# Performance work log

Measured on AMD Instinct MI355X. Metric: run time of the kernel, lower is better.

The kernel has to match this reference:

```python
import jax, jax.numpy as jnp
import numpy as np

N = 50000      # nodes
CI = 256       # multiplicity of irreps_in  (256x0e + 256x1o)
CH = 128       # multiplicity of irreps_hidden (128x0e + 128x1o)
INV_SQRT3 = 0.5773502691896258  # CG norm for 1o x 1o -> 0e (dot)


def _split(x, C):
    # e3nn layout: [scalars (C), vectors (C*3, per-channel m-contiguous)]
    return x[:, :C], x[:, C:].reshape(x.shape[0], C, 3)


def _normgate(s, v, w1, b1, w2, b2):
    # QHNet NormGate: concat(scalars, per-channel vector norms) -> MLP -> gates
    norms = jnp.sqrt(jnp.sum(v * v, axis=-1))                      # [N, Cv]
    g = jax.nn.silu(jnp.concatenate([s, norms], 1) @ w1 + b1) @ w2 + b2
    Cs = s.shape[1]
    return jax.nn.silu(g[:, :Cs]), v * g[:, Cs:, None]


def _o3linear(s, v, W0, b0, W1):
    # per-irrep block-diagonal linear, e3nn fan-in normalization; bias only on 0e
    inv = 1.0 / np.sqrt(s.shape[1]).astype(np.float32)
    return s @ W0 * inv + b0, jnp.einsum('nui,uh->nhi', v, W1) * inv


def _forward(x, fcl1_w, fcl1_b, fcl2_w, fcl2_b, fcr1_w, fcr1_b, fcr2_w, fcr2_b,
             fcp1_w, fcp1_b, fcp2_w, fcp2_b, Wl0, bl0, Wl1, Wr0, br0, Wr1,
             Wp0, bp0, Wp1, w_ss, w_sv, w_vs, w_vv):
    s, v = _split(x, CI)                                           # [N,CI],[N,CI,3]
    # left / right branches: NormGate -> o3.Linear (irreps_in -> irreps_hidden)
    ls, lv = _normgate(s, v, fcl1_w, fcl1_b, fcl2_w, fcl2_b)
    ls, lv = _o3linear(ls, lv, Wl0, bl0, Wl1)                      # [N,CH],[N,CH,3]
    rs, rv = _normgate(s, v, fcr1_w, fcr1_b, fcr2_w, fcr2_b)
    rs, rv = _o3linear(rs, rv, Wr0, br0, Wr1)
    # channelwise ('uuu') CG tensor product with internal per-channel weights
    # paths: 0e*0e->0e, 1o.1o->0e, 0e*1o->1o, 1o*0e->1o
    s_a = w_ss * ls * rs
    s_b = w_vv * jnp.sum(lv * rv, -1) * INV_SQRT3
    v_a = w_sv[None, :, None] * ls[:, :, None] * rv
    v_b = w_vs[None, :, None] * lv * rs[:, :, None]
    tp_s = jnp.concatenate([s_a, s_b], 1)                          # [N, 2*CH]
    tp_v = jnp.concatenate([v_a, v_b], 1)                          # [N, 2*CH, 3]
    # residual update (irreps_tp_out == irreps_in by construction)
    tp_s = tp_s + s
    tp_v = tp_v + v
    # output gate + projection to hidden irreps
    ps, pv = _normgate(tp_s, tp_v, fcp1_w, fcp1_b, fcp2_w, fcp2_b)
    ps, pv = _o3linear(ps, pv, Wp0, bp0, Wp1)                      # [N,CH],[N,CH,3]
    return jnp.concatenate([ps, pv.reshape(pv.shape[0], -1)], 1)   # [N, 4*CH]


def setup_inputs():
    key = jax.random.key(0)
    ks = jax.random.split(key, 24)
    M = 2 * CI  # total multiplicity of irreps_in / irreps_tp_out (NormGate fc width)

    def lin(k, fi, fo):
        return jax.random.normal(k, (fi, fo), jnp.float32) / np.sqrt(fi)

    inp = {"x": jax.random.normal(ks[0], (N, 4 * CI), jnp.float32)}
    i = 1
    for nm in ["fcl", "fcr", "fcp"]:
        inp[nm + "1_w"] = lin(ks[i], M, M); i += 1
        inp[nm + "1_b"] = jnp.zeros((M,), jnp.float32)
        inp[nm + "2_w"] = lin(ks[i], M, M); i += 1
        inp[nm + "2_b"] = jnp.zeros((M,), jnp.float32)
    for nm in ["Wl", "Wr", "Wp"]:
        inp[nm + "0"] = jax.random.normal(ks[i], (CI, CH), jnp.float32); i += 1
        inp["b" + nm[1] + "0"] = jnp.zeros((CH,), jnp.float32)
        inp[nm + "1"] = jax.random.normal(ks[i], (CI, CH), jnp.float32); i += 1
    for nm in ["w_ss", "w_sv", "w_vs", "w_vv"]:
        inp[nm] = jax.random.normal(ks[i], (CH,), jnp.float32); i += 1
    return inp


def reference(x, fcl1_w, fcl1_b, fcl2_w, fcl2_b, fcr1_w, fcr1_b, fcr2_w, fcr2_b,
              fcp1_w, fcp1_b, fcp2_w, fcp2_b, Wl0, bl0, Wl1, Wr0, br0, Wr1,
              Wp0, bp0, Wp1, w_ss, w_sv, w_vs, w_vv):
    return _forward(x, fcl1_w, fcl1_b, fcl2_w, fcl2_b, fcr1_w, fcr1_b, fcr2_w,
                    fcr2_b, fcp1_w, fcp1_b, fcp2_w, fcp2_b, Wl0, bl0, Wl1, Wr0,
                    br0, Wr1, Wp0, bp0, Wp1, w_ss, w_sv, w_vs, w_vv)
```

## Files before the change

kernel.cpp:

```cpp
#include <hip/hip_runtime.h>
#include <cstddef>

#define NN 50000
#define NP 50048
#define RT 391

typedef unsigned short u16;
typedef __attribute__((ext_vector_type(8))) short bf16x8;
typedef __attribute__((ext_vector_type(4))) float f32x4;

__device__ __forceinline__ float bf2f(u16 h){
  union { unsigned u; float f; } x; x.u = ((unsigned)h) << 16; return x.f;
}
__device__ __forceinline__ u16 f2bf(float f){
  union { float f; unsigned u; } x; x.f = f;
  unsigned r = x.u + 0x7fffu + ((x.u >> 16) & 1u);
  return (u16)(r >> 16);
}
__device__ __forceinline__ float silu_f(float v){
  return v / (1.f + __expf(-v));
}
__device__ __forceinline__ void gll16(const u16* g, u16* l){
  __builtin_amdgcn_global_load_lds(
      (const __attribute__((address_space(1))) unsigned int*)g,
      (__attribute__((address_space(3))) unsigned int*)l, 16, 0, 0);
}
__device__ __forceinline__ int xcd_swz(int hw, int nblk){
  int q = nblk >> 3, r = nblk & 7;
  int xcd = hw & 7, j = hw >> 3;
  return (xcd < r ? xcd*(q+1) : r*(q+1) + (xcd - r)*q) + j;
}
#define SWZ(row) (((row) >> 1) & 3)

__global__ __launch_bounds__(256)
void k_wt(const float* b0,const float* b1,const float* b2,const float* b3,
          const float* b4,const float* b5,
          const float* s0,const float* s1,const float* s2,const float* s3,
          const float* s4,const float* s5, u16* __restrict__ dst){
  __shared__ float t[64][68];
  const int m = blockIdx.y;
  const bool big = (m < 6);
  const int K = big ? 512 : 256, C = big ? 512 : 128;
  const int tC = C >> 6;
  const int tiles = (K >> 6) * tC;
  if((int)blockIdx.x >= tiles) return;
  const int k0 = ((int)blockIdx.x / tC) << 6, c0 = ((int)blockIdx.x % tC) << 6;
  const float* src = m==0?b0:m==1?b1:m==2?b2:m==3?b3:m==4?b4:m==5?b5:
                     m==6?s0:m==7?s1:m==8?s2:m==9?s3:m==10?s4:s5;
  u16* d = dst + (big ? (size_t)m*262144 : (size_t)(6*262144) + (size_t)(m-6)*32768);
  const int tr = threadIdx.x >> 2, tc = (threadIdx.x & 3) << 4;
  const float* sp = src + (size_t)(k0 + tr)*C + c0 + tc;
#pragma unroll
  for(int j=0;j<16;j+=4) *(f32x4*)&t[tr][tc + j] = *(const f32x4*)(sp + j);
  __syncthreads();
  u16* dp = d + (size_t)(c0 + tr)*K + k0 + tc;
#pragma unroll
  for(int j=0;j<16;j++) dp[j] = f2bf(t[tc + j][tr]);
}

__global__ __launch_bounds__(256)
void k_prep(const float* __restrict__ x, u16* __restrict__ A0,
            u16* __restrict__ XVp){
  const int n = blockIdx.x;
  const int t = threadIdx.x;
  u16* row = A0 + (size_t)n * 512;
  u16* xv  = XVp + (size_t)n * 768;
  if(n >= NN){
    row[t] = 0; row[256 + t] = 0;
    xv[t] = 0; xv[256 + t] = 0; xv[512 + t] = 0;
    return;
  }
  const float* xr = x + (size_t)n * 1024;
  row[t] = f2bf(xr[t]);
  float a = xr[256 + 3*t], b = xr[256 + 3*t + 1], c = xr[256 + 3*t + 2];
  row[256 + t] = f2bf(sqrtf(a*a + b*b + c*c));
  xv[t] = f2bf(a); xv[256 + t] = f2bf(b); xv[512 + t] = f2bf(c);
}

template<int K, int RING>
__device__ __forceinline__ void gemm_core(const u16* __restrict__ A, int lda,
                                          const u16* __restrict__ Bt, int ldb,
                                          u16* lds, f32x4 acc[4][4]){
  constexpr int NT = K / 32;
  static_assert(NT >= RING, "");
  const int tid  = threadIdx.x;
  const int lane = tid & 63;
  const int wid  = tid >> 6;
  const int wm = (wid >> 1) << 6;
  const int wn = (wid & 1) << 6;
  const int lr = lane & 15;
  const int lh = lane >> 4;
#pragma unroll
  for(int mi=0;mi<4;mi++)
#pragma unroll
    for(int ni=0;ni<4;ni++) acc[mi][ni] = (f32x4)(0.f);

  const int r0 = tid >> 2, s0 = tid & 3, r1 = (tid + 256) >> 2;
  const u16* agA0 = A  + (size_t)r0*lda + (size_t)((s0 ^ SWZ(r0)) * 8);
  const u16* agA1 = A  + (size_t)r1*lda + (size_t)((s0 ^ SWZ(r1)) * 8);
  const u16* agB0 = Bt + (size_t)r0*ldb + (size_t)((s0 ^ SWZ(r0)) * 8);
  const u16* agB1 = Bt + (size_t)r1*ldb + (size_t)((s0 ^ SWZ(r1)) * 8);

#define STAGE(b, k0)                                         \
  { u16* lbase = lds + (size_t)(b) * 8192;                   \
    gll16(agA0 + (k0), lbase + tid*8);                       \
    gll16(agA1 + (k0), lbase + (tid+256)*8);                 \
    gll16(agB0 + (k0), lbase + 4096 + tid*8);                \
    gll16(agB1 + (k0), lbase + 4096 + (tid+256)*8); }

#pragma unroll
  for(int p=0;p<RING-1;p++) STAGE(p, p*32)

  int cur = 0, nxt = RING - 1;
  for(int kt = 0; kt < NT; ++kt){
    if constexpr      (RING == 5) asm volatile("s_waitcnt vmcnt(12)" ::: "memory");
    else if constexpr (RING == 4) asm volatile("s_waitcnt vmcnt(8)"  ::: "memory");
    else                          asm volatile("s_waitcnt vmcnt(4)"  ::: "memory");
    __builtin_amdgcn_s_barrier();
    {
      int kf = kt + RING - 1; if(kf > NT-1) kf = NT-1;
      STAGE(nxt, kf*32)
    }
    const u16* la = lds + (size_t)cur * 8192;
    const u16* lb = la + 4096;
    bf16x8 af[4], bv[4];
#pragma unroll
    for(int i=0;i<4;i++){
      const int ra = wm + i*16 + lr;
      af[i] = *(const bf16x8*)(la + ra*32 + ((lh ^ SWZ(ra)) * 8));
      const int rb = wn + i*16 + lr;
      bv[i] = *(const bf16x8*)(lb + rb*32 + ((lh ^ SWZ(rb)) * 8));
    }
    __builtin_amdgcn_s_setprio(1);
#pragma unroll
    for(int mi=0;mi<4;mi++)
#pragma unroll
      for(int ni=0;ni<4;ni++)
        acc[mi][ni] = __builtin_amdgcn_mfma_f32_16x16x32_bf16(
                          af[mi], bv[ni], acc[mi][ni], 0, 0, 0);
    __builtin_amdgcn_s_setprio(0);
    cur = (cur == RING-1) ? 0 : cur + 1;
    nxt = (nxt == RING-1) ? 0 : nxt + 1;
  }
#undef STAGE
  asm volatile("s_waitcnt vmcnt(0)" ::: "memory");
  __builtin_amdgcn_s_barrier();
}

__device__ __forceinline__ void cstage_write(u16* lds, int rl, int cl, float v){
  const int b = ((rl << 8) + (cl << 1)) ^ ((rl & 7) << 4);
  *(u16*)((char*)lds + b) = f2bf(v);
}
__device__ __forceinline__ bf16x8 cstage_read(const u16* lds, int rl, int cl){
  const int b = ((rl << 8) + (cl << 1)) ^ ((rl & 7) << 4);
  return *(const bf16x8*)((const char*)lds + b);
}

template<int EPI, int NZ>
__global__ __launch_bounds__(256, 3)
void k_fc(const u16* __restrict__ Al, const u16* __restrict__ Ar,
          const u16* __restrict__ Btl, const u16* __restrict__ Btr,
          const float* __restrict__ bl, const float* __restrict__ br_,
          u16* __restrict__ ol, u16* __restrict__ orr,
          const u16* __restrict__ gsrc){
  __shared__ u16 lds[24576];
  const int nblk = RT * 4 * NZ;
  const int L = xcd_swz(blockIdx.x, nblk);
  int rowTileI, colTileI, z;
  if(NZ == 2){ rowTileI = L >> 3; int sub = L & 7; colTileI = sub >> 1; z = sub & 1; }
  else       { rowTileI = L >> 2; colTileI = L & 3; z = 0; }
  const u16* A  = z ? Ar  : Al;
  const u16* Bt = z ? Btr : Btl;
  const float* bias = z ? br_ : bl;
  u16* o = z ? orr : ol;
  const int tileRow = rowTileI << 7;
  const int colTile = colTileI << 7;
  f32x4 acc[4][4];
  gemm_core<512,3>(A + (size_t)tileRow*512, 512, Bt + (size_t)colTile*512, 512,
                   lds, acc);
  const int tid = threadIdx.x, lane = tid & 63, wid = tid >> 6;
  const int wm=(wid>>1)<<6, wn=(wid&1)<<6, lr=lane&15, lh=lane>>4;
  const bool gateTile = (EPI != 0) && (colTile >= 256);
#pragma unroll
  for(int mi=0;mi<4;mi++){
#pragma unroll
    for(int ni=0;ni<4;ni++){
      const int cl = wn + ni*16 + lr;
      const float bv = bias[colTile + cl];
#pragma unroll
      for(int r=0;r<4;r++){
        const int rl = wm + mi*16 + lh*4 + r;
        float v = acc[mi][ni][r] + bv;
        if(!gateTile) v = silu_f(v);
        cstage_write(lds, rl, cl, v);
      }
    }
  }
  __syncthreads();
  if(!gateTile){
    const int ldo = (EPI == 0) ? 512 : 1024;
#pragma unroll
    for(int j=0;j<8;j++){
      const int q = j*256 + tid;
      const int row = q >> 4, slot = q & 15;
      bf16x8 v = cstage_read(lds, row, slot*8);
      *(bf16x8*)(o + (size_t)(tileRow + row)*ldo + colTile + slot*8) = v;
    }
  } else {
    const int ub = colTile - 256;
#pragma unroll 4
    for(int j=0;j<24;j++){
      const int q = j*256 + tid;
      const int row = q / 48, w = q - row*48;
      const int pl = w >> 4, slot = w & 15;
      const int n = tileRow + row;
      bf16x8 g8 = cstage_read(lds, row, slot*8);
      bf16x8 x8 = *(const bf16x8*)(gsrc + (size_t)n*768 + pl*256 + ub + slot*8);
      bf16x8 o8;
#pragma unroll
      for(int e=0;e<8;e++)
        o8[e] = (short)f2bf(bf2f((u16)x8[e]) * bf2f((u16)g8[e]));
      *(bf16x8*)(o + (size_t)n*1024 + 256 + pl*256 + ub + slot*8) = o8;
    }
  }
}

template<int EPI>
__global__ __launch_bounds__(256, 3)
void k_o3(const u16* __restrict__ AL, const u16* __restrict__ AR,
          const u16* __restrict__ W0L, const u16* __restrict__ W1L,
          const u16* __restrict__ W0R, const u16* __restrict__ W1R,
          const float* __restrict__ bL, const float* __restrict__ bR,
          u16* __restrict__ oL, u16* __restrict__ oR,
          float* __restrict__ fout, float* __restrict__ PVp){
  __shared__ u16 lds[24576];
  const int nblk = RT * ((EPI==0) ? 8 : 4);
  const int L = xcd_swz(blockIdx.x, nblk);
  int rowTileI, br, comp;
  if(EPI == 0){ rowTileI = L >> 3; int sub = L & 7; br = sub >> 2; comp = sub & 3; }
  else        { rowTileI = L >> 2; comp = L & 3; br = 0; }
  const u16* A  = br ? AR : AL;
  const u16* Bt = br ? (comp ? W1R : W0R) : (comp ? W1L : W0L);
  const float* bias = br ? bR : bL;
  u16* o16 = br ? oR : oL;
  const int aoff = comp ? (256 + (comp-1)*256) : 0;
  const int tileRow = rowTileI << 7;
  f32x4 acc[4][4];
  gemm_core<256,3>(A + (size_t)tileRow*1024 + aoff, 1024, Bt, 256, lds, acc);
  const int tid = threadIdx.x, lane = tid & 63, wid = tid >> 6;
  const int wm=(wid>>1)<<6, wn=(wid&1)<<6, lr=lane&15, lh=lane>>4;
  if(EPI == 0){
#pragma unroll
    for(int mi=0;mi<4;mi++){
#pragma unroll
      for(int ni=0;ni<4;ni++){
        const int cl = wn + ni*16 + lr;
#pragma unroll
        for(int r=0;r<4;r++){
          const int rl = wm + mi*16 + lh*4 + r;
          float v = acc[mi][ni][r] * 0.0625f;
          if(comp == 0) v += bias[cl];
          cstage_write(lds, rl, cl, v);
        }
      }
    }
    __syncthreads();
#pragma unroll
    for(int j=0;j<8;j++){
      const int q = j*256 + tid;
      const int row = q >> 4, slot = q & 15;
      bf16x8 v = cstage_read(lds, row, slot*8);
      *(bf16x8*)(o16 + (size_t)(tileRow + row)*512 + comp*128 + slot*8) = v;
    }
  } else {
    float* lf = (float*)lds;
#pragma unroll
    for(int half=0; half<2; ++half){
      if((wm >> 6) == half){
#pragma unroll
        for(int mi=0;mi<4;mi++){
#pragma unroll
          for(int ni=0;ni<4;ni++){
            const int cl = wn + ni*16 + lr;
#pragma unroll
            for(int r=0;r<4;r++){
              const int rl = mi*16 + lh*4 + r;
              float v = acc[mi][ni][r] * 0.0625f;
              if(comp == 0) v += bias[cl];
              const int b = (rl*512 + cl*4) ^ ((rl & 7) << 4);
              *(float*)((char*)lf + b) = v;
            }
          }
        }
      }
      __syncthreads();
#pragma unroll
      for(int j=0;j<8;j++){
        const int q = j*256 + tid;
        const int row = q >> 5, slot = q & 31;
        const int n = tileRow + half*64 + row;
        const int b = (row*512 + slot*16) ^ ((row & 7) << 4);
        f32x4 v = *(const f32x4*)((const char*)lf + b);
        if(n < NN){
          if(comp == 0) *(f32x4*)(fout + (size_t)n*512 + slot*4) = v;
          else *(f32x4*)(PVp + (size_t)n*384 + (size_t)(comp-1)*128 + slot*4) = v;
        }
      }
      __syncthreads();
    }
  }
}

__global__ __launch_bounds__(256)
void k_out(const float* __restrict__ PVp, float* __restrict__ out){
  const int n = (blockIdx.x << 1) + (threadIdx.x >> 7);
  if(n >= NN) return;
  const int c = threadIdx.x & 127;
  const float* s = PVp + (size_t)n*384 + c;
  const float v0 = s[0], v1 = s[128], v2 = s[256];
  float* d = out + (size_t)n*512 + 128 + c*3;
  d[0] = v0; d[1] = v1; d[2] = v2;
}

__global__ __launch_bounds__(256)
void k_tp(const u16* __restrict__ OL, const u16* __restrict__ ORr,
          const u16* __restrict__ XVpp,
          const float* __restrict__ w_ss, const float* __restrict__ w_sv,
          const float* __restrict__ w_vs, const float* __restrict__ w_vv,
          u16* A2, u16* __restrict__ TPV){
  const int n = (blockIdx.x << 1) + (threadIdx.x >> 7);
  const int h = threadIdx.x & 127;
  const u16* ol  = OL  + (size_t)n * 512;
  const u16* orv = ORr + (size_t)n * 512;
  const float ls = bf2f(ol[h]),  rs = bf2f(orv[h]);
  const float lv0=bf2f(ol[128+h]),  lv1=bf2f(ol[256+h]),  lv2=bf2f(ol[384+h]);
  const float rv0=bf2f(orv[128+h]), rv1=bf2f(orv[256+h]), rv2=bf2f(orv[384+h]);
  const float wss=w_ss[h], wsv=w_sv[h], wvs=w_vs[h], wvv=w_vv[h];
  float sa = wss * ls * rs;
  float sb = wvv * (lv0*rv0 + lv1*rv1 + lv2*rv2) * 0.5773502691896258f;
  float va0 = wsv*ls*rv0, va1 = wsv*ls*rv1, va2 = wsv*ls*rv2;
  float vb0 = wvs*lv0*rs, vb1 = wvs*lv1*rs, vb2 = wvs*lv2*rs;
  if(n < NN){
    const u16* a0 = A2 + (size_t)n * 512;
    const u16* xv = XVpp + (size_t)n * 768;
    sa += bf2f(a0[h]); sb += bf2f(a0[128 + h]);
    va0 += bf2f(xv[h]);       va1 += bf2f(xv[256 + h]);  va2 += bf2f(xv[512 + h]);
    vb0 += bf2f(xv[128 + h]); vb1 += bf2f(xv[384 + h]);  vb2 += bf2f(xv[640 + h]);
  }
  u16* a2 = A2 + (size_t)n * 512;
  a2[h]       = f2bf(sa);
  a2[128 + h] = f2bf(sb);
  a2[256 + h] = f2bf(sqrtf(va0*va0 + va1*va1 + va2*va2));
  a2[384 + h] = f2bf(sqrtf(vb0*vb0 + vb1*vb1 + vb2*vb2));
  u16* tv = TPV + (size_t)n * 768;
  tv[h]       = f2bf(va0);  tv[128 + h] = f2bf(vb0);
  tv[256 + h] = f2bf(va1);  tv[384 + h] = f2bf(vb1);
  tv[512 + h] = f2bf(va2);  tv[640 + h] = f2bf(vb2);
}

extern "C" void kernel_launch(void* const* d_in, const int* in_sizes, int n_in,
                              void* d_out, int out_size, void* d_ws, size_t ws_size,
                              hipStream_t stream){
  const float* x      = (const float*)d_in[0];
  const float* fcl1_w = (const float*)d_in[1];  const float* fcl1_b = (const float*)d_in[2];
  const float* fcl2_w = (const float*)d_in[3];  const float* fcl2_b = (const float*)d_in[4];
  const float* fcr1_w = (const float*)d_in[5];  const float* fcr1_b = (const float*)d_in[6];
  const float* fcr2_w = (const float*)d_in[7];  const float* fcr2_b = (const float*)d_in[8];
  const float* fcp1_w = (const float*)d_in[9];  const float* fcp1_b = (const float*)d_in[10];
  const float* fcp2_w = (const float*)d_in[11]; const float* fcp2_b = (const float*)d_in[12];
  const float* Wl0 = (const float*)d_in[13]; const float* bl0 = (const float*)d_in[14];
  const float* Wl1 = (const float*)d_in[15];
  const float* Wr0 = (const float*)d_in[16]; const float* br0 = (const float*)d_in[17];
  const float* Wr1 = (const float*)d_in[18];
  const float* Wp0 = (const float*)d_in[19]; const float* bp0 = (const float*)d_in[20];
  const float* Wp1 = (const float*)d_in[21];
  const float* w_ss = (const float*)d_in[22]; const float* w_sv = (const float*)d_in[23];
  const float* w_vs = (const float*)d_in[24]; const float* w_vv = (const float*)d_in[25];
  float* out = (float*)d_out;

  u16* WT = (u16*)d_ws;
  u16* wt_fcl1 = WT + 0*262144;
  u16* wt_fcl2 = WT + 1*262144;
  u16* wt_fcr1 = WT + 2*262144;
  u16* wt_fcr2 = WT + 3*262144;
  u16* wt_fcp1 = WT + 4*262144;
  u16* wt_fcp2 = WT + 5*262144;
  u16* wt_sm  = WT + 6*262144;
  u16* wt_Wl0 = wt_sm + 0*32768;
  u16* wt_Wl1 = wt_sm + 1*32768;
  u16* wt_Wr0 = wt_sm + 2*32768;
  u16* wt_Wr1 = wt_sm + 3*32768;
  u16* wt_Wp0 = wt_sm + 4*32768;
  u16* wt_Wp1 = wt_sm + 5*32768;
  char* base = (char*)d_ws;
  const size_t SZ512  = (size_t)NP * 512 * 2;
  const size_t SZ1024 = (size_t)NP * 1024 * 2;
  const size_t W_RES  = (size_t)4 << 20;
  u16* A0 = (u16*)(base + W_RES);
  u16* Hl = (u16*)(base + W_RES + 1*SZ512);
  u16* Hr = (u16*)(base + W_RES + 2*SZ512);
  u16* BL = (u16*)(base + W_RES + 3*SZ512);
  u16* BR = (u16*)(base + W_RES + 3*SZ512 + SZ1024);
  u16* XVp = (u16*)d_out;
  float* PVp = (float*)BL;
  (void)ws_size; (void)in_sizes; (void)n_in; (void)out_size;

  k_wt<<<dim3(64,12), 256, 0, stream>>>(fcl1_w, fcl2_w, fcr1_w, fcr2_w, fcp1_w, fcp2_w,
                                        Wl0, Wl1, Wr0, Wr1, Wp0, Wp1, WT);
  k_prep<<<NP, 256, 0, stream>>>(x, A0, XVp);
  k_fc<0,2><<<RT*8, 256, 0, stream>>>(A0, A0, wt_fcl1, wt_fcr1,
                                      fcl1_b, fcr1_b, Hl, Hr, nullptr);
  k_fc<1,2><<<RT*8, 256, 0, stream>>>(Hl, Hr, wt_fcl2, wt_fcr2,
                                      fcl2_b, fcr2_b, BL, BR, XVp);
  k_o3<0><<<RT*8, 256, 0, stream>>>(BL, BR, wt_Wl0, wt_Wl1, wt_Wr0, wt_Wr1,
                                    bl0, br0, Hl, Hr, nullptr, nullptr);
  k_tp<<<NP/2, 256, 0, stream>>>(Hl, Hr, XVp, w_ss, w_sv, w_vs, w_vv, A0, BL);
  k_fc<0,1><<<RT*4, 256, 0, stream>>>(A0, A0, wt_fcp1, wt_fcp1,
                                      fcp1_b, fcp1_b, Hl, Hl, nullptr);
  k_fc<2,1><<<RT*4, 256, 0, stream>>>(Hl, Hl, wt_fcp2, wt_fcp2,
                                      fcp2_b, fcp2_b, BR, BR, BL);
  k_o3<1><<<RT*4, 256, 0, stream>>>(BR, BR, wt_Wp0, wt_Wp1, nullptr, nullptr,
                                    bp0, bp0, nullptr, nullptr, out, PVp);
  k_out<<<NN/2, 256, 0, stream>>>(PVp, out);
}
```

Before: 631.5 us.

## Enlarge GEMM tile to 256x128 with 4x1 warp layout

The shared GEMM core now uses 256-row tiles (each wave owns 64 rows by all 128 columns) instead of 128x128, with a fixed 3-stage LDS ring of 24 KB stages. This halves the number of row tiles, which raises B-fragment reuse per A load and cuts redundant weight traffic. Each wave now holds 32 accumulators. In exchange the kernels drop occupancy from 3 to 2 blocks per CU, use more registers and LDS, and pad rows further (NP 50176).

Measured after the change: 682.0 us. +8.0%, slower.

```diff
diff --git a/kernel.cpp b/kernel.cpp
--- a/kernel.cpp
+++ b/kernel.cpp
@@ -2,8 +2,8 @@
 #include <cstddef>
 
 #define NN 50000
-#define NP 50048
-#define RT 391
+#define NP 50176
+#define RTM 196
 
 typedef unsigned short u16;
 typedef __attribute__((ext_vector_type(8))) short bf16x8;
@@ -77,70 +77,69 @@
   xv[t] = f2bf(a); xv[256 + t] = f2bf(b); xv[512 + t] = f2bf(c);
 }
 
-template<int K, int RING>
+template<int K>
 __device__ __forceinline__ void gemm_core(const u16* __restrict__ A, int lda,
                                           const u16* __restrict__ Bt, int ldb,
-                                          u16* lds, f32x4 acc[4][4]){
+                                          u16* lds, f32x4 acc[4][8]){
   constexpr int NT = K / 32;
-  static_assert(NT >= RING, "");
+  static_assert(NT >= 3, "");
   const int tid  = threadIdx.x;
   const int lane = tid & 63;
   const int wid  = tid >> 6;
-  const int wm = (wid >> 1) << 6;
-  const int wn = (wid & 1) << 6;
   const int lr = lane & 15;
   const int lh = lane >> 4;
 #pragma unroll
   for(int mi=0;mi<4;mi++)
 #pragma unroll
-    for(int ni=0;ni<4;ni++) acc[mi][ni] = (f32x4)(0.f);
-
-  const int r0 = tid >> 2, s0 = tid & 3, r1 = (tid + 256) >> 2;
-  const u16* agA0 = A  + (size_t)r0*lda + (size_t)((s0 ^ SWZ(r0)) * 8);
-  const u16* agA1 = A  + (size_t)r1*lda + (size_t)((s0 ^ SWZ(r1)) * 8);
-  const u16* agB0 = Bt + (size_t)r0*ldb + (size_t)((s0 ^ SWZ(r0)) * 8);
-  const u16* agB1 = Bt + (size_t)r1*ldb + (size_t)((s0 ^ SWZ(r1)) * 8);
-
-#define STAGE(b, k0)                                         \
-  { u16* lbase = lds + (size_t)(b) * 8192;                   \
-    gll16(agA0 + (k0), lbase + tid*8);                       \
-    gll16(agA1 + (k0), lbase + (tid+256)*8);                 \
-    gll16(agB0 + (k0), lbase + 4096 + tid*8);                \
-    gll16(agB1 + (k0), lbase + 4096 + (tid+256)*8); }
-
-#pragma unroll
-  for(int p=0;p<RING-1;p++) STAGE(p, p*32)
-
-  int cur = 0, nxt = RING - 1;
+    for(int ni=0;ni<8;ni++) acc[mi][ni] = (f32x4)(0.f);
+
+  const int r_ = tid >> 2, s_ = tid & 3;
+  const u16* agA[4];
+  const u16* agB[2];
+#pragma unroll
+  for(int i=0;i<4;i++){ int row = r_ + i*64; agA[i] = A  + (size_t)row*lda + (size_t)((s_ ^ SWZ(row))*8); }
+#pragma unroll
+  for(int i=0;i<2;i++){ int row = r_ + i*64; agB[i] = Bt + (size_t)row*ldb + (size_t)((s_ ^ SWZ(row))*8); }
+
+#define STAGE(b, k0)                                                   \
+  { u16* lb_ = lds + (size_t)(b) * 12288;                              \
+    _Pragma("unroll") for(int i_=0;i_<4;i_++)                          \
+      gll16(agA[i_] + (k0), lb_ + (tid + i_*256)*8);                   \
+    _Pragma("unroll") for(int i_=0;i_<2;i_++)                          \
+      gll16(agB[i_] + (k0), lb_ + 8192 + (tid + i_*256)*8); }
+
+  STAGE(0, 0) STAGE(1, 32)
+  int cur = 0, nxt = 2;
   for(int kt = 0; kt < NT; ++kt){
-    if constexpr      (RING == 5) asm volatile("s_waitcnt vmcnt(12)" ::: "memory");
-    else if constexpr (RING == 4) asm volatile("s_waitcnt vmcnt(8)"  ::: "memory");
-    else                          asm volatile("s_waitcnt vmcnt(4)"  ::: "memory");
+    asm volatile("s_waitcnt vmcnt(6)" ::: "memory");
     __builtin_amdgcn_s_barrier();
     {
-      int kf = kt + RING - 1; if(kf > NT-1) kf = NT-1;
+      int kf = kt + 2; if(kf > NT-1) kf = NT-1;
       STAGE(nxt, kf*32)
     }
-    const u16* la = lds + (size_t)cur * 8192;
-    const u16* lb = la + 4096;
-    bf16x8 af[4], bv[4];
+    const u16* la = lds + (size_t)cur * 12288;
+    const u16* lb = la + 8192;
+    bf16x8 af[4], bv[8];
 #pragma unroll
     for(int i=0;i<4;i++){
-      const int ra = wm + i*16 + lr;
+      const int ra = wid*64 + i*16 + lr;
       af[i] = *(const bf16x8*)(la + ra*32 + ((lh ^ SWZ(ra)) * 8));
-      const int rb = wn + i*16 + lr;
+    }
+#pragma unroll
+    for(int i=0;i<8;i++){
+      const int rb = i*16 + lr;
       bv[i] = *(const bf16x8*)(lb + rb*32 + ((lh ^ SWZ(rb)) * 8));
     }
     __builtin_amdgcn_s_setprio(1);
 #pragma unroll
     for(int mi=0;mi<4;mi++)
 #pragma unroll
-      for(int ni=0;ni<4;ni++)
+      for(int ni=0;ni<8;ni++)
         acc[mi][ni] = __builtin_amdgcn_mfma_f32_16x16x32_bf16(
                           af[mi], bv[ni], acc[mi][ni], 0, 0, 0);
     __builtin_amdgcn_s_setprio(0);
-    cur = (cur == RING-1) ? 0 : cur + 1;
-    nxt = (nxt == RING-1) ? 0 : nxt + 1;
+    cur = (cur == 2) ? 0 : cur + 1;
+    nxt = (nxt == 2) ? 0 : nxt + 1;
   }
 #undef STAGE
   asm volatile("s_waitcnt vmcnt(0)" ::: "memory");
@@ -157,14 +156,14 @@
 }
 
 template<int EPI, int NZ>
-__global__ __launch_bounds__(256, 3)
+__global__ __launch_bounds__(256, 2)
 void k_fc(const u16* __restrict__ Al, const u16* __restrict__ Ar,
           const u16* __restrict__ Btl, const u16* __restrict__ Btr,
           const float* __restrict__ bl, const float* __restrict__ br_,
           u16* __restrict__ ol, u16* __restrict__ orr,
           const u16* __restrict__ gsrc){
-  __shared__ u16 lds[24576];
-  const int nblk = RT * 4 * NZ;
+  __shared__ u16 lds[36864];
+  const int nblk = RTM * 4 * NZ;
   const int L = xcd_swz(blockIdx.x, nblk);
   int rowTileI, colTileI, z;
   if(NZ == 2){ rowTileI = L >> 3; int sub = L & 7; colTileI = sub >> 1; z = sub & 1; }
@@ -173,23 +172,23 @@
   const u16* Bt = z ? Btr : Btl;
   const float* bias = z ? br_ : bl;
   u16* o = z ? orr : ol;
-  const int tileRow = rowTileI << 7;
+  const int tileRow = rowTileI << 8;
   const int colTile = colTileI << 7;
-  f32x4 acc[4][4];
-  gemm_core<512,3>(A + (size_t)tileRow*512, 512, Bt + (size_t)colTile*512, 512,
-                   lds, acc);
+  f32x4 acc[4][8];
+  gemm_core<512>(A + (size_t)tileRow*512, 512, Bt + (size_t)colTile*512, 512,
+                 lds, acc);
   const int tid = threadIdx.x, lane = tid & 63, wid = tid >> 6;
-  const int wm=(wid>>1)<<6, wn=(wid&1)<<6, lr=lane&15, lh=lane>>4;
+  const int lr = lane & 15, lh = lane >> 4;
   const bool gateTile = (EPI != 0) && (colTile >= 256);
 #pragma unroll
   for(int mi=0;mi<4;mi++){
 #pragma unroll
-    for(int ni=0;ni<4;ni++){
-      const int cl = wn + ni*16 + lr;
+    for(int ni=0;ni<8;ni++){
+      const int cl = ni*16 + lr;
       const float bv = bias[colTile + cl];
 #pragma unroll
       for(int r=0;r<4;r++){
-        const int rl = wm + mi*16 + lh*4 + r;
+        const int rl = wid*64 + mi*16 + lh*4 + r;
         float v = acc[mi][ni][r] + bv;
         if(!gateTile) v = silu_f(v);
         cstage_write(lds, rl, cl, v);
@@ -200,7 +199,7 @@
   if(!gateTile){
     const int ldo = (EPI == 0) ? 512 : 1024;
 #pragma unroll
-    for(int j=0;j<8;j++){
+    for(int j=0;j<16;j++){
       const int q = j*256 + tid;
       const int row = q >> 4, slot = q & 15;
       bf16x8 v = cstage_read(lds, row, slot*8);
@@ -209,7 +208,7 @@
   } else {
     const int ub = colTile - 256;
 #pragma unroll 4
-    for(int j=0;j<24;j++){
+    for(int j=0;j<48;j++){
       const int q = j*256 + tid;
       const int row = q / 48, w = q - row*48;
       const int pl = w >> 4, slot = w & 15;
@@ -226,15 +225,15 @@
 }
 
 template<int EPI>
-__global__ __launch_bounds__(256, 3)
+__global__ __launch_bounds__(256, 2)
 void k_o3(const u16* __restrict__ AL, const u16* __restrict__ AR,
           const u16* __restrict__ W0L, const u16* __restrict__ W1L,
           const u16* __restrict__ W0R, const u16* __restrict__ W1R,
           const float* __restrict__ bL, const float* __restrict__ bR,
           u16* __restrict__ oL, u16* __restrict__ oR,
           float* __restrict__ fout, float* __restrict__ PVp){
-  __shared__ u16 lds[24576];
-  const int nblk = RT * ((EPI==0) ? 8 : 4);
+  __shared__ u16 lds[36864];
+  const int nblk = RTM * ((EPI==0) ? 8 : 4);
   const int L = xcd_swz(blockIdx.x, nblk);
   int rowTileI, br, comp;
   if(EPI == 0){ rowTileI = L >> 3; int sub = L & 7; br = sub >> 2; comp = sub & 3; }
@@ -244,20 +243,20 @@
   const float* bias = br ? bR : bL;
   u16* o16 = br ? oR : oL;
   const int aoff = comp ? (256 + (comp-1)*256) : 0;
-  const int tileRow = rowTileI << 7;
-  f32x4 acc[4][4];
-  gemm_core<256,3>(A + (size_t)tileRow*1024 + aoff, 1024, Bt, 256, lds, acc);
+  const int tileRow = rowTileI << 8;
+  f32x4 acc[4][8];
+  gemm_core<256>(A + (size_t)tileRow*1024 + aoff, 1024, Bt, 256, lds, acc);
   const int tid = threadIdx.x, lane = tid & 63, wid = tid >> 6;
-  const int wm=(wid>>1)<<6, wn=(wid&1)<<6, lr=lane&15, lh=lane>>4;
+  const int lr = lane & 15, lh = lane >> 4;
   if(EPI == 0){
 #pragma unroll
     for(int mi=0;mi<4;mi++){
 #pragma unroll
-      for(int ni=0;ni<4;ni++){
-        const int cl = wn + ni*16 + lr;
+      for(int ni=0;ni<8;ni++){
+        const int cl = ni*16 + lr;
 #pragma unroll
         for(int r=0;r<4;r++){
-          const int rl = wm + mi*16 + lh*4 + r;
+          const int rl = wid*64 + mi*16 + lh*4 + r;
           float v = acc[mi][ni][r] * 0.0625f;
           if(comp == 0) v += bias[cl];
           cstage_write(lds, rl, cl, v);
@@ -266,7 +265,7 @@
     }
     __syncthreads();
 #pragma unroll
-    for(int j=0;j<8;j++){
+    for(int j=0;j<16;j++){
       const int q = j*256 + tid;
       const int row = q >> 4, slot = q & 15;
       bf16x8 v = cstage_read(lds, row, slot*8);
@@ -276,15 +275,15 @@
     float* lf = (float*)lds;
 #pragma unroll
     for(int half=0; half<2; ++half){
-      if((wm >> 6) == half){
+      if((wid >> 1) == half){
 #pragma unroll
         for(int mi=0;mi<4;mi++){
 #pragma unroll
-          for(int ni=0;ni<4;ni++){
-            const int cl = wn + ni*16 + lr;
+          for(int ni=0;ni<8;ni++){
+            const int cl = ni*16 + lr;
 #pragma unroll
             for(int r=0;r<4;r++){
-              const int rl = mi*16 + lh*4 + r;
+              const int rl = (wid&1)*64 + mi*16 + lh*4 + r;
               float v = acc[mi][ni][r] * 0.0625f;
               if(comp == 0) v += bias[cl];
               const int b = (rl*512 + cl*4) ^ ((rl & 7) << 4);
@@ -295,10 +294,10 @@
       }
       __syncthreads();
 #pragma unroll
-      for(int j=0;j<8;j++){
+      for(int j=0;j<16;j++){
         const int q = j*256 + tid;
         const int row = q >> 5, slot = q & 31;
-        const int n = tileRow + half*64 + row;
+        const int n = tileRow + half*128 + row;
         const int b = (row*512 + slot*16) ^ ((row & 7) << 4);
         f32x4 v = *(const f32x4*)((const char*)lf + b);
         if(n < NN){
@@ -408,18 +407,18 @@
   k_wt<<<dim3(64,12), 256, 0, stream>>>(fcl1_w, fcl2_w, fcr1_w, fcr2_w, fcp1_w, fcp2_w,
                                         Wl0, Wl1, Wr0, Wr1, Wp0, Wp1, WT);
   k_prep<<<NP, 256, 0, stream>>>(x, A0, XVp);
-  k_fc<0,2><<<RT*8, 256, 0, stream>>>(A0, A0, wt_fcl1, wt_fcr1,
-                                      fcl1_b, fcr1_b, Hl, Hr, nullptr);
-  k_fc<1,2><<<RT*8, 256, 0, stream>>>(Hl, Hr, wt_fcl2, wt_fcr2,
-                                      fcl2_b, fcr2_b, BL, BR, XVp);
-  k_o3<0><<<RT*8, 256, 0, stream>>>(BL, BR, wt_Wl0, wt_Wl1, wt_Wr0, wt_Wr1,
-                                    bl0, br0, Hl, Hr, nullptr, nullptr);
+  k_fc<0,2><<<RTM*8, 256, 0, stream>>>(A0, A0, wt_fcl1, wt_fcr1,
+                                       fcl1_b, fcr1_b, Hl, Hr, nullptr);
+  k_fc<1,2><<<RTM*8, 256, 0, stream>>>(Hl, Hr, wt_fcl2, wt_fcr2,
+                                       fcl2_b, fcr2_b, BL, BR, XVp);
+  k_o3<0><<<RTM*8, 256, 0, stream>>>(BL, BR, wt_Wl0, wt_Wl1, wt_Wr0, wt_Wr1,
+                                     bl0, br0, Hl, Hr, nullptr, nullptr);
   k_tp<<<NP/2, 256, 0, stream>>>(Hl, Hr, XVp, w_ss, w_sv, w_vs, w_vv, A0, BL);
-  k_fc<0,1><<<RT*4, 256, 0, stream>>>(A0, A0, wt_fcp1, wt_fcp1,
-                                      fcp1_b, fcp1_b, Hl, Hl, nullptr);
-  k_fc<2,1><<<RT*4, 256, 0, stream>>>(Hl, Hl, wt_fcp2, wt_fcp2,
-                                      fcp2_b, fcp2_b, BR, BR, BL);
-  k_o3<1><<<RT*4, 256, 0, stream>>>(BR, BR, wt_Wp0, wt_Wp1, nullptr, nullptr,
-                                    bp0, bp0, nullptr, nullptr, out, PVp);
+  k_fc<0,1><<<RTM*4, 256, 0, stream>>>(A0, A0, wt_fcp1, wt_fcp1,
+                                       fcp1_b, fcp1_b, Hl, Hl, nullptr);
+  k_fc<2,1><<<RTM*4, 256, 0, stream>>>(Hl, Hl, wt_fcp2, wt_fcp2,
+                                       fcp2_b, fcp2_b, BR, BR, BL);
+  k_o3<1><<<RTM*4, 256, 0, stream>>>(BR, BR, wt_Wp0, wt_Wp1, nullptr, nullptr,
+                                     bp0, bp0, nullptr, nullptr, out, PVp);
   k_out<<<NN/2, 256, 0, stream>>>(PVp, out);
 }
```

## Shrink GEMM LDS ring to double buffer to fit four blocks per CU

Applied to the files above, without the earlier changes.

Replaces the three-stage global-to-LDS prefetch ring with a two-stage double buffer and cuts shared memory per block from 48KB to 32KB. Launch bounds go from 3 to 4 blocks per CU, aiming for higher occupancy. The fp32 epilogue in k_o3 is split into four 32-row quarters so it fits the smaller LDS. The cost is less latency hiding: each k-step now waits on vmcnt(0), so every load must land before compute, and the extra 32-row epilogue passes add barriers.

After: 610.5 us (median of 2 runs). -3.3%, faster.

```diff
diff --git a/kernel.cpp b/kernel.cpp
--- a/kernel.cpp
+++ b/kernel.cpp
@@ -77,12 +77,12 @@
   xv[t] = f2bf(a); xv[256 + t] = f2bf(b); xv[512 + t] = f2bf(c);
 }
 
-template<int K, int RING>
+template<int K>
 __device__ __forceinline__ void gemm_core(const u16* __restrict__ A, int lda,
                                           const u16* __restrict__ Bt, int ldb,
                                           u16* lds, f32x4 acc[4][4]){
   constexpr int NT = K / 32;
-  static_assert(NT >= RING, "");
+  static_assert(NT >= 2, "");
   const int tid  = threadIdx.x;
   const int lane = tid & 63;
   const int wid  = tid >> 6;
@@ -108,18 +108,14 @@
     gll16(agB0 + (k0), lbase + 4096 + tid*8);                \
     gll16(agB1 + (k0), lbase + 4096 + (tid+256)*8); }
 
-#pragma unroll
-  for(int p=0;p<RING-1;p++) STAGE(p, p*32)
-
-  int cur = 0, nxt = RING - 1;
+  STAGE(0, 0)
   for(int kt = 0; kt < NT; ++kt){
-    if constexpr      (RING == 5) asm volatile("s_waitcnt vmcnt(12)" ::: "memory");
-    else if constexpr (RING == 4) asm volatile("s_waitcnt vmcnt(8)"  ::: "memory");
-    else                          asm volatile("s_waitcnt vmcnt(4)"  ::: "memory");
+    const int cur = kt & 1;
+    asm volatile("s_waitcnt vmcnt(0)" ::: "memory");
     __builtin_amdgcn_s_barrier();
     {
-      int kf = kt + RING - 1; if(kf > NT-1) kf = NT-1;
-      STAGE(nxt, kf*32)
+      int kf = kt + 1; if(kf > NT-1) kf = NT-1;
+      STAGE(cur ^ 1, kf*32)
     }
     const u16* la = lds + (size_t)cur * 8192;
     const u16* lb = la + 4096;
@@ -139,8 +135,6 @@
         acc[mi][ni] = __builtin_amdgcn_mfma_f32_16x16x32_bf16(
                           af[mi], bv[ni], acc[mi][ni], 0, 0, 0);
     __builtin_amdgcn_s_setprio(0);
-    cur = (cur == RING-1) ? 0 : cur + 1;
-    nxt = (nxt == RING-1) ? 0 : nxt + 1;
   }
 #undef STAGE
   asm volatile("s_waitcnt vmcnt(0)" ::: "memory");
@@ -157,13 +151,13 @@
 }
 
 template<int EPI, int NZ>
-__global__ __launch_bounds__(256, 3)
+__global__ __launch_bounds__(256, 4)
 void k_fc(const u16* __restrict__ Al, const u16* __restrict__ Ar,
           const u16* __restrict__ Btl, const u16* __restrict__ Btr,
           const float* __restrict__ bl, const float* __restrict__ br_,
           u16* __restrict__ ol, u16* __restrict__ orr,
           const u16* __restrict__ gsrc){
-  __shared__ u16 lds[24576];
+  __shared__ u16 lds[16384];
   const int nblk = RT * 4 * NZ;
   const int L = xcd_swz(blockIdx.x, nblk);
   int rowTileI, colTileI, z;
@@ -176,8 +170,8 @@
   const int tileRow = rowTileI << 7;
   const int colTile = colTileI << 7;
   f32x4 acc[4][4];
-  gemm_core<512,3>(A + (size_t)tileRow*512, 512, Bt + (size_t)colTile*512, 512,
-                   lds, acc);
+  gemm_core<512>(A + (size_t)tileRow*512, 512, Bt + (size_t)colTile*512, 512,
+                 lds, acc);
   const int tid = threadIdx.x, lane = tid & 63, wid = tid >> 6;
   const int wm=(wid>>1)<<6, wn=(wid&1)<<6, lr=lane&15, lh=lane>>4;
   const bool gateTile = (EPI != 0) && (colTile >= 256);
@@ -226,14 +220,14 @@
 }
 
 template<int EPI>
-__global__ __launch_bounds__(256, 3)
+__global__ __launch_bounds__(256, 4)
 void k_o3(const u16* __restrict__ AL, const u16* __restrict__ AR,
           const u16* __restrict__ W0L, const u16* __restrict__ W1L,
           const u16* __restrict__ W0R, const u16* __restrict__ W1R,
           const float* __restrict__ bL, const float* __restrict__ bR,
           u16* __restrict__ oL, u16* __restrict__ oR,
           float* __restrict__ fout, float* __restrict__ PVp){
-  __shared__ u16 lds[24576];
+  __shared__ u16 lds[16384];
   const int nblk = RT * ((EPI==0) ? 8 : 4);
   const int L = xcd_swz(blockIdx.x, nblk);
   int rowTileI, br, comp;
@@ -246,7 +240,7 @@
   const int aoff = comp ? (256 + (comp-1)*256) : 0;
   const int tileRow = rowTileI << 7;
   f32x4 acc[4][4];
-  gemm_core<256,3>(A + (size_t)tileRow*1024 + aoff, 1024, Bt, 256, lds, acc);
+  gemm_core<256>(A + (size_t)tileRow*1024 + aoff, 1024, Bt, 256, lds, acc);
   const int tid = threadIdx.x, lane = tid & 63, wid = tid >> 6;
   const int wm=(wid>>1)<<6, wn=(wid&1)<<6, lr=lane&15, lh=lane>>4;
   if(EPI == 0){
@@ -275,16 +269,17 @@
   } else {
     float* lf = (float*)lds;
 #pragma unroll
-    for(int half=0; half<2; ++half){
-      if((wm >> 6) == half){
-#pragma unroll
-        for(int mi=0;mi<4;mi++){
+    for(int qu=0; qu<4; ++qu){
+      const int mi0 = (qu & 1) * 2;
+      if((wm >> 6) == (qu >> 1)){
+#pragma unroll
+        for(int mi=mi0; mi<mi0+2; mi++){
 #pragma unroll
           for(int ni=0;ni<4;ni++){
             const int cl = wn + ni*16 + lr;
 #pragma unroll
             for(int r=0;r<4;r++){
-              const int rl = mi*16 + lh*4 + r;
+              const int rl = (mi - mi0)*16 + lh*4 + r;
               float v = acc[mi][ni][r] * 0.0625f;
               if(comp == 0) v += bias[cl];
               const int b = (rl*512 + cl*4) ^ ((rl & 7) << 4);
@@ -295,10 +290,10 @@
       }
       __syncthreads();
 #pragma unroll
-      for(int j=0;j<8;j++){
+      for(int j=0;j<4;j++){
         const int q = j*256 + tid;
         const int row = q >> 5, slot = q & 31;
-        const int n = tileRow + half*64 + row;
+        const int n = tileRow + qu*32 + row;
         const int b = (row*512 + slot*16) ^ ((row & 7) << 4);
         f32x4 v = *(const f32x4*)((const char*)lf + b);
         if(n < NN){
```
